# Kernel optimization log

Measured on AMD Instinct MI355X. Metric: run time of the kernel, lower is better.

The kernel has to match this reference:

```python
import jax, jax.numpy as jnp
import numpy as np

A = -0.75  # torch grid_sample bicubic coefficient
EPS_CLAMP = 1e-07


def geo_pad(x, p):
    # GeoCyclicPadding: flip+half-roll across poles (H), circular in longitude (W)
    B, C, H, W = x.shape
    top = jnp.roll(jnp.flip(x[:, :, :p, :], axis=2), W // 2, axis=3)
    bot = jnp.roll(jnp.flip(x[:, :, H - p:, :], axis=2), W // 2, axis=3)
    x = jnp.concatenate([top, x, bot], axis=2)
    return jnp.concatenate([x[:, :, :, W - p:], x, x[:, :, :, :p]], axis=3)


def conv3(x, w, b):
    y = jax.lax.conv_general_dilated(x, w, (1, 1), 'VALID',
                                     dimension_numbers=('NCHW', 'OIHW', 'NCHW'))
    return y + b[None, :, None, None]


def layernorm_chw(x, g, b):
    mu = jnp.mean(x, axis=(1, 2, 3), keepdims=True)
    var = jnp.mean((x - mu) ** 2, axis=(1, 2, 3), keepdims=True)
    return (x - mu) * jax.lax.rsqrt(var + 1e-5) * g[None] + b[None]


def cubic_weights(t):
    # cubic convolution weights for taps at offsets -1,0,1,2 (a = -0.75)
    w0 = A * (1 + t) ** 3 - 5 * A * (1 + t) ** 2 + 8 * A * (1 + t) - 4 * A
    w1 = (A + 2) * t ** 3 - (A + 3) * t ** 2 + 1
    w2 = (A + 2) * (1 - t) ** 3 - (A + 3) * (1 - t) ** 2 + 1
    w3 = A * (2 - t) ** 3 - 5 * A * (2 - t) ** 2 + 8 * A * (2 - t) - 4 * A
    return (w0, w1, w2, w3)


def bicubic_sample_border(img, gx, gy):
    # img: [N,Hp,Wp]; gx,gy: [N,H,W] normalized coords; align_corners=True, border padding
    N, Hp, Wp = img.shape
    ix = jnp.clip((gx + 1) * 0.5 * (Wp - 1), 0.0, Wp - 1)
    iy = jnp.clip((gy + 1) * 0.5 * (Hp - 1), 0.0, Hp - 1)
    x0f = jnp.floor(ix)
    y0f = jnp.floor(iy)
    tx = ix - x0f
    ty = iy - y0f
    x0 = x0f.astype(jnp.int32)
    y0 = y0f.astype(jnp.int32)
    wx = cubic_weights(tx)
    wy = cubic_weights(ty)
    nidx = jnp.arange(N)[:, None, None]
    out = jnp.zeros_like(ix)
    for i in range(4):
        yi = jnp.clip(y0 + (i - 1), 0, Hp - 1)
        row = jnp.zeros_like(ix)
        for j in range(4):
            xj = jnp.clip(x0 + (j - 1), 0, Wp - 1)
            row = row + wx[j] * img[nidx, yi, xj]
        out = out + wy[i] * row
    return out


def reference(hidden_features, lat_grid, lon_grid, w1, b1, ln_g, ln_b, w2, b2, dt):
    B, C, H, W = hidden_features.shape
    # velocity_net = CLP (double conv)
    x = geo_pad(hidden_features, 1)
    x = conv3(x, w1, b1)
    x = jax.nn.silu(layernorm_chw(x, ln_g, ln_b))
    x = geo_pad(x, 1)
    vel = conv3(x, w2, b2)                      # [B, 2C, H, W]
    vel = vel.reshape(B, 2, C, H, W).transpose(0, 2, 1, 3, 4)  # [B, C, 2, H, W]
    u = vel[:, :, 0]
    v = vel[:, :, 1]
    lon_prime = -u * dt
    lat_prime = -v * dt
    lat_p = lat_grid[:, None, :, :]  # broadcast over channels
    lon_p = lon_grid[:, None, :, :]
    # rotated -> standard lat/lon
    sin_lat_prime = jnp.sin(lat_prime)
    cos_lat_prime = jnp.cos(lat_prime)
    sin_lon_prime = jnp.sin(lon_prime)
    cos_lon_prime = jnp.cos(lon_prime)
    sin_lat_p = jnp.sin(lat_p)
    cos_lat_p = jnp.cos(lat_p)
    sin_lat = sin_lat_prime * cos_lat_p + cos_lat_prime * cos_lon_prime * sin_lat_p
    lat_dep = jnp.arcsin(jnp.clip(sin_lat, -1 + EPS_CLAMP, 1 - EPS_CLAMP))
    num = cos_lat_prime * sin_lon_prime
    den = cos_lat_prime * cos_lon_prime * cos_lat_p - sin_lat_prime * sin_lat_p
    lon_dep = lon_p + jnp.arctan2(num, den)
    lon_dep = jnp.remainder(lon_dep + 2 * jnp.pi, 2 * jnp.pi)
    pw = W + 2
    ph = H + 2
    grid_x = (lon_dep / (2 * jnp.pi) * 2 - 1) * (W / pw)
    grid_y = (lat_dep / jnp.pi * 2 - 1) * (H / ph)
    padded = geo_pad(hidden_features, 1).reshape(B * C, ph, pw)
    out = bicubic_sample_border(padded,
                                grid_x.reshape(B * C, H, W),
                                grid_y.reshape(B * C, H, W))
    return out.reshape(B, C, H, W)


def setup_inputs() -> dict:
    key = jax.random.key(0)
    ks = jax.random.split(key, 4)
    B, C, H, W = 2, 128, 240, 480
    hidden_features = jax.random.normal(ks[0], (B, C, H, W), dtype=jnp.float32)
    lat = jnp.linspace(-jnp.pi / 2 + 1e-3, jnp.pi / 2 - 1e-3, H, dtype=jnp.float32)
    lon = jnp.linspace(0.0, 2 * jnp.pi * (1 - 1.0 / W), W, dtype=jnp.float32)
    lat_grid = jnp.broadcast_to(lat[None, :, None], (B, H, W)).astype(jnp.float32)
    lon_grid = jnp.broadcast_to(lon[None, None, :], (B, H, W)).astype(jnp.float32)
    w1 = jax.random.normal(ks[1], (C, C, 3, 3), dtype=jnp.float32) * 0.02
    b1 = jnp.zeros((C,), dtype=jnp.float32)
    ln_g = jnp.ones((C, H, W), dtype=jnp.float32)
    ln_b = jnp.zeros((C, H, W), dtype=jnp.float32)
    w2 = jax.random.normal(ks[2], (2 * C, C, 3, 3), dtype=jnp.float32) * 0.02
    b2 = jnp.zeros((2 * C,), dtype=jnp.float32)
    return {"hidden_features": hidden_features, "lat_grid": lat_grid,
            "lon_grid": lon_grid, "w1": w1, "b1": b1, "ln_g": ln_g,
            "ln_b": ln_b, "w2": w2, "b2": b2, "dt": 0.1}
```

## Files before the change

### kernel.cpp

```cpp
#include <hip/hip_runtime.h>
#include <math.h>

#define Hh 240
#define Ww 480
#define HW 115200
#define Cc 128
#define Kk 1152
#define HALFW 240
#define NB_RED 1440
#define WLCAP 4194304

typedef unsigned int u32;
typedef unsigned short u16;
typedef short bf16x8 __attribute__((ext_vector_type(8)));
typedef float f32x4 __attribute__((ext_vector_type(4)));
typedef __attribute__((address_space(3))) u32 lds_u32;
typedef const __attribute__((address_space(1))) u32 glb_u32;

__device__ __forceinline__ u16 f2bf(float x) {
    u32 u = __float_as_uint(x);
    u32 r = (u + 0x7fffu + ((u >> 16) & 1u)) >> 16;
    return (u16)r;
}
__device__ __forceinline__ float bf2f(u16 h) { return __uint_as_float(((u32)h) << 16); }

__device__ __forceinline__ int geo_sidx(int r, int c) {
    int wv = (c < 0) ? (Ww - 1) : ((c >= Ww) ? 0 : c);
    int rr;
    if (r < 0)        { rr = 0;      wv = (wv >= HALFW) ? wv - HALFW : wv + HALFW; }
    else if (r >= Hh) { rr = Hh - 1; wv = (wv >= HALFW) ? wv - HALFW : wv + HALFW; }
    else              { rr = r; }
    return rr * Ww + wv;
}

__device__ __forceinline__ float padfetch(const float* __restrict__ p, int yi, int xj) {
    return p[geo_sidx(yi - 1, xj - 1)];
}

__device__ __forceinline__ void sincos_small(double x, double* s, double* c) {
    double x2 = x * x;
    if (x2 > 0.49) { *s = sin(x); *c = cos(x); return; }
    *s = x * (1.0 + x2 * (-1.6666666666666666e-1 + x2 * (8.3333333333333333e-3 +
         x2 * (-1.9841269841269841e-4 + x2 * (2.7557319223985893e-6 - x2 * 2.5052108385441720e-8)))));
    *c = 1.0 + x2 * (-0.5 + x2 * (4.1666666666666666e-2 + x2 * (-1.3888888888888889e-3 +
         x2 * (2.4801587301587302e-5 - x2 * 2.7557319223985893e-7))));
}

__device__ __forceinline__ void snipe_tail(double u, double v, double dt,
                                           double phi_s, double phi_c, double lam,
                                           const float* __restrict__ plane,
                                           float* __restrict__ outp)
{
    const double TWO_PI = 6.2831853071795864769252867665590;
    const double PI_D   = 3.1415926535897932384626433832795;

    double lonp = -u * dt, latp = -v * dt;
    double slp, clp, slo, clo;
    sincos_small(latp, &slp, &clp);
    sincos_small(lonp, &slo, &clo);

    double sinlat = slp * phi_c + clp * clo * phi_s;
    sinlat = fmin(fmax(sinlat, -1.0 + 1e-7), 1.0 - 1e-7);
    double lat_dep = asin(sinlat);

    double num = clp * slo;
    double den = clp * clo * phi_c - slp * phi_s;
    double lon_dep = lam + atan2(num, den);
    double xr = lon_dep + TWO_PI;
    xr = xr - floor(xr / TWO_PI) * TWO_PI;

    double gx = (xr / TWO_PI * 2.0 - 1.0) * (480.0 / 482.0);
    double gy = (lat_dep / PI_D * 2.0 - 1.0) * (240.0 / 242.0);
    double ixd = fmin(fmax((gx + 1.0) * 0.5 * 481.0, 0.0), 481.0);
    double iyd = fmin(fmax((gy + 1.0) * 0.5 * 241.0, 0.0), 241.0);

    double x0d = floor(ixd), y0d = floor(iyd);
    float fx = (float)(ixd - x0d), fy = (float)(iyd - y0d);
    int x0 = (int)x0d, y0 = (int)y0d;

    const float a = -0.75f;
    float wx[4], wy[4];
    {
        float t = fx;
        float t1 = 1.f + t, t2 = 2.f - t, s1 = 1.f - t;
        wx[0] = ((a * t1 - 5.f * a) * t1 + 8.f * a) * t1 - 4.f * a;
        wx[1] = ((a + 2.f) * t - (a + 3.f)) * t * t + 1.f;
        wx[2] = ((a + 2.f) * s1 - (a + 3.f)) * s1 * s1 + 1.f;
        wx[3] = ((a * t2 - 5.f * a) * t2 + 8.f * a) * t2 - 4.f * a;
        t = fy;
        t1 = 1.f + t; t2 = 2.f - t; s1 = 1.f - t;
        wy[0] = ((a * t1 - 5.f * a) * t1 + 8.f * a) * t1 - 4.f * a;
        wy[1] = ((a + 2.f) * t - (a + 3.f)) * t * t + 1.f;
        wy[2] = ((a + 2.f) * s1 - (a + 3.f)) * s1 * s1 + 1.f;
        wy[3] = ((a * t2 - 5.f * a) * t2 + 8.f * a) * t2 - 4.f * a;
    }
    float accv = 0.f;
    #pragma unroll
    for (int i = 0; i < 4; i++) {
        int yi = min(max(y0 + i - 1, 0), 241);
        float row = 0.f;
        #pragma unroll
        for (int j = 0; j < 4; j++) {
            int xj = min(max(x0 + j - 1, 0), 481);
            row = fmaf(wx[j], padfetch(plane, yi, xj), row);
        }
        accv = fmaf(wy[i], row, accv);
    }
    *outp = accv;
}

__global__ void reorder_w(const float* __restrict__ w, u16* __restrict__ outp, int NN) {
    int idx = blockIdx.x * 256 + threadIdx.x;
    int total = 3 * NN * Kk;
    if (idx >= total) return;
    int per_kt = 3 * NN * 32;
    int t = idx / per_kt;
    int rem = idx - t * per_kt;
    int U = rem >> 3, j = rem & 7;
    int NT64 = (NN / 16) * 64;
    int p = U / NT64;
    int r2 = U - p * NT64;
    int ntile = r2 >> 6, part = (r2 >> 4) & 3, nlow = r2 & 15;
    int n = ntile * 16 + nlow;
    int k = t * 32 + part * 8 + j;
    float x = w[(size_t)n * Kk + k];
    u16 a = f2bf(x); float r1 = x - bf2f(a);
    u16 b = f2bf(r1); float rr = r1 - bf2f(b);
    outp[idx] = (p == 0) ? a : ((p == 1) ? b : f2bf(rr));
}

template<int NN>
__global__ __launch_bounds__(256)
void conv_mfma(const float* __restrict__ in,
               const u16*  __restrict__ wspr,
               const float* __restrict__ bias,
               float* __restrict__ out)
{
    constexpr int NT     = NN / 32;
    constexpr int NTILES = NN / 16;
    __shared__ short Al[3][8][4][16][8];
    __shared__ short Bl[3][NTILES][4][16][8];

    const int tid  = threadIdx.x;
    const int lane = tid & 63;
    const int wave = tid >> 6;
    const int wm = wave & 1, wn = wave >> 1;
    const int lr = lane & 15, kg = lane >> 4;
    const int m0 = blockIdx.x * 128;

    const int ms   = tid & 127;
    const int ks   = (tid >> 7) * 16;
    const int mt_s = ms >> 4, lr_s = ms & 15;
    const int kg0  = ks >> 3;
    const int gm = m0 + ms;
    const int h = gm / Ww, w = gm - h * Ww;
    int sidx[9];
    #pragma unroll
    for (int q = 0; q < 9; q++) sidx[q] = geo_sidx(h + q / 3 - 1, w + q % 3 - 1);

    short* const Blbase = &Bl[0][0][0][0][0];
    const u16* const bsrc = wspr + (size_t)tid * 8;
    constexpr int NCH = (3 * NN * 32 / 8) / 256;

    f32x4 acc[4][NT] = {};

    for (int kt = 0; kt < Kk; kt += 32) {
        __syncthreads();
        {
            const u16* src = bsrc + (size_t)(kt >> 5) * (3 * NN * 32);
            #pragma unroll
            for (int cg = 0; cg < NCH; cg++) {
                __builtin_amdgcn_global_load_lds(
                    (glb_u32*)(src + (size_t)cg * 2048),
                    (lds_u32*)(Blbase + (size_t)(cg * 256 + tid) * 8),
                    16, 0, 0);
            }
        }
        {
            int k = kt + ks;
            int ic = k / 9, t9 = k - ic * 9;
            short hh[3][16];
            #pragma unroll
            for (int j = 0; j < 16; j++) {
                float x = in[ic * HW + sidx[t9]];
                u16 a = f2bf(x); float r1 = x - bf2f(a);
                u16 b = f2bf(r1); float r2 = r1 - bf2f(b);
                hh[0][j] = (short)a; hh[1][j] = (short)b; hh[2][j] = (short)f2bf(r2);
                if (++t9 == 9) { t9 = 0; ic++; }
            }
            #pragma unroll
            for (int p = 0; p < 3; p++) {
                #pragma unroll
                for (int half = 0; half < 2; half++) {
                    bf16x8 v;
                    #pragma unroll
                    for (int j = 0; j < 8; j++) v[j] = hh[p][half * 8 + j];
                    *(bf16x8*)&Al[p][mt_s][kg0 + half][lr_s][0] = v;
                }
            }
        }
        __syncthreads();
        bf16x8 af[3][4];
        #pragma unroll
        for (int pa = 0; pa < 3; pa++)
            #pragma unroll
            for (int mt = 0; mt < 4; mt++)
                af[pa][mt] = *(const bf16x8*)&Al[pa][wm * 4 + mt][kg][lr][0];
        #pragma unroll
        for (int pb = 0; pb < 3; pb++) {
            #pragma unroll
            for (int nt = 0; nt < NT; nt++) {
                bf16x8 bq = *(const bf16x8*)&Bl[pb][wn * NT + nt][kg][lr][0];
                #pragma unroll
                for (int pa = 0; pa < 3 - pb; pa++) {
                    #pragma unroll
                    for (int mt = 0; mt < 4; mt++)
                        acc[mt][nt] = __builtin_amdgcn_mfma_f32_16x16x32_bf16(
                            af[pa][mt], bq, acc[mt][nt], 0, 0, 0);
                }
            }
        }
    }
    #pragma unroll
    for (int mt = 0; mt < 4; mt++) {
        int mbase = m0 + wm * 64 + mt * 16 + kg * 4;
        #pragma unroll
        for (int nt = 0; nt < NT; nt++) {
            int n = wn * (NN / 2) + nt * 16 + lr;
            float bv = bias[n];
            float4 o;
            o.x = acc[mt][nt][0] + bv;
            o.y = acc[mt][nt][1] + bv;
            o.z = acc[mt][nt][2] + bv;
            o.w = acc[mt][nt][3] + bv;
            *(float4*)&out[(size_t)n * HW + mbase] = o;
        }
    }
}

__global__ __launch_bounds__(256)
void reduce_stats(const float* __restrict__ y, float* __restrict__ part) {
    const int n4 = (Cc * HW) / 4;
    float s = 0.f, ss = 0.f;
    for (int i = blockIdx.x * 256 + threadIdx.x; i < n4; i += NB_RED * 256) {
        float4 v = ((const float4*)y)[i];
        s  += v.x + v.y + v.z + v.w;
        ss += v.x * v.x + v.y * v.y + v.z * v.z + v.w * v.w;
    }
    #pragma unroll
    for (int o = 32; o > 0; o >>= 1) { s += __shfl_down(s, o); ss += __shfl_down(ss, o); }
    __shared__ float ls[4], lss[4];
    int wid = threadIdx.x >> 6, lane = threadIdx.x & 63;
    if (lane == 0) { ls[wid] = s; lss[wid] = ss; }
    __syncthreads();
    if (threadIdx.x == 0) {
        part[blockIdx.x * 2]     = ls[0] + ls[1] + ls[2] + ls[3];
        part[blockIdx.x * 2 + 1] = lss[0] + lss[1] + lss[2] + lss[3];
    }
}

__global__ __launch_bounds__(256)
void finalize_stats(const float* __restrict__ part, float* __restrict__ stats) {
    float s = 0.f, ss = 0.f;
    for (int i = threadIdx.x; i < NB_RED; i += 256) { s += part[2 * i]; ss += part[2 * i + 1]; }
    #pragma unroll
    for (int o = 32; o > 0; o >>= 1) { s += __shfl_down(s, o); ss += __shfl_down(ss, o); }
    __shared__ float ls[4], lss[4];
    int wid = threadIdx.x >> 6, lane = threadIdx.x & 63;
    if (lane == 0) { ls[wid] = s; lss[wid] = ss; }
    __syncthreads();
    if (threadIdx.x == 0) {
        stats[0] = ls[0] + ls[1] + ls[2] + ls[3];
        stats[1] = lss[0] + lss[1] + lss[2] + lss[3];
    }
}

__global__ void norm_silu(float* __restrict__ y, const float* __restrict__ g,
                          const float* __restrict__ bb, const float* __restrict__ stats) {
    int i = blockIdx.x * 256 + threadIdx.x;
    if (i >= Cc * HW) return;
    const float invN = 1.f / (float)(Cc * HW);
    float mu  = stats[0] * invN;
    float var = stats[1] * invN - mu * mu;
    float inv = rsqrtf(var + 1e-5f);
    float z = (y[i] - mu) * inv * g[i] + bb[i];
    y[i] = z / (1.f + expf(-z));
}

__global__ __launch_bounds__(256)
void semilag(const float* __restrict__ vel, const float* __restrict__ hid,
             const float* __restrict__ latg, const float* __restrict__ lng,
             const float* __restrict__ dtp, float* __restrict__ out,
             u32* __restrict__ wl, u32* __restrict__ wlcnt)
{
    int idx = blockIdx.x * 256 + threadIdx.x;
    if (idx >= Cc * HW) return;
    int c = idx / HW;
    int m = idx - c * HW;

    const float PI2F = 6.28318530717958647692f;

    float uf = vel[idx];
    float vf = vel[Cc * HW + idx];
    float dtf = dtp[0];
    float phi = latg[m], lam = lng[m];
    float sphi = sinf(phi), cphi = cosf(phi);

    float lonp = -uf * dtf, latp = -vf * dtf;
    float slp = sinf(latp), clp = cosf(latp);
    float slo = sinf(lonp), clo = cosf(lonp);
    float sinlat = slp * cphi + clp * clo * sphi;
    float num = clp * slo;
    float den = clp * clo * cphi - slp * sphi;
    float r2 = num * num + den * den;

    float lon_w = lam + atan2f(num, den) + PI2F;
    lon_w = lon_w - floorf(lon_w / PI2F) * PI2F;
    float seam = fminf(lon_w, PI2F - lon_w);

    bool pole = (m < 2 * Ww) | (m >= HW - 2 * Ww);
    bool snipe = !pole & ((r2 < 1e-4f) | (fabsf(sinlat) > 1.f - 1e-5f) | (seam < 1e-3f));
    if (snipe) {
        u32 s = atomicAdd(wlcnt, 1u);
        if (s < WLCAP) wl[s] = (u32)idx;
    }

    float sl = fminf(fmaxf(sinlat, -1.f + 1e-7f), 1.f - 1e-7f);
    float lat_dep = asinf(sl);
    float gx = (lon_w / PI2F * 2.f - 1.f) * (480.f / 482.f);
    float gy = (lat_dep / 3.14159265358979323846f * 2.f - 1.f) * (240.f / 242.f);
    double ixd = (double)fminf(fmaxf((gx + 1.f) * 0.5f * 481.f, 0.f), 481.f);
    double iyd = (double)fminf(fmaxf((gy + 1.f) * 0.5f * 241.f, 0.f), 241.f);

    double x0d = floor(ixd), y0d = floor(iyd);
    float fx = (float)(ixd - x0d), fy = (float)(iyd - y0d);
    int x0 = (int)x0d, y0 = (int)y0d;

    const float a = -0.75f;
    float wx[4], wy[4];
    {
        float t = fx;
        float t1 = 1.f + t, t2 = 2.f - t, s1 = 1.f - t;
        wx[0] = ((a * t1 - 5.f * a) * t1 + 8.f * a) * t1 - 4.f * a;
        wx[1] = ((a + 2.f) * t - (a + 3.f)) * t * t + 1.f;
        wx[2] = ((a + 2.f) * s1 - (a + 3.f)) * s1 * s1 + 1.f;
        wx[3] = ((a * t2 - 5.f * a) * t2 + 8.f * a) * t2 - 4.f * a;
        t = fy;
        t1 = 1.f + t; t2 = 2.f - t; s1 = 1.f - t;
        wy[0] = ((a * t1 - 5.f * a) * t1 + 8.f * a) * t1 - 4.f * a;
        wy[1] = ((a + 2.f) * t - (a + 3.f)) * t * t + 1.f;
        wy[2] = ((a + 2.f) * s1 - (a + 3.f)) * s1 * s1 + 1.f;
        wy[3] = ((a * t2 - 5.f * a) * t2 + 8.f * a) * t2 - 4.f * a;
    }

    const float* plane = hid + (size_t)c * HW;
    float accv = 0.f;
    #pragma unroll
    for (int i = 0; i < 4; i++) {
        int yi = min(max(y0 + i - 1, 0), 241);
        float row = 0.f;
        #pragma unroll
        for (int j = 0; j < 4; j++) {
            int xj = min(max(x0 + j - 1, 0), 481);
            row = fmaf(wx[j], padfetch(plane, yi, xj), row);
        }
        accv = fmaf(wy[i], row, accv);
    }
    out[idx] = accv;
}

__global__ __launch_bounds__(256)
void sniper_rows(const float* __restrict__ y1, const float* __restrict__ w2,
                 const float* __restrict__ b2, const float* __restrict__ hid,
                 const float* __restrict__ latg, const float* __restrict__ lng,
                 const float* __restrict__ dtp, float* __restrict__ out)
{
    __shared__ float xl[Kk];
    __shared__ double resd[256];

    const int tid = threadIdx.x;
    const int ri  = blockIdx.x / Ww;
    const int col = blockIdx.x - ri * Ww;
    const int r   = (ri < 2) ? ri : (236 + ri);
    const int m   = r * Ww + col;

    for (int k = tid; k < Kk; k += 256) {
        int ic = k / 9, t9 = k - ic * 9;
        xl[k] = y1[ic * HW + geo_sidx(r + t9 / 3 - 1, col + t9 % 3 - 1)];
    }
    __syncthreads();

    {
        const float* wrow = w2 + (size_t)tid * Kk;
        double a0 = 0.0, a1 = 0.0, a2 = 0.0, a3 = 0.0;
        #pragma unroll 4
        for (int k = 0; k < Kk; k += 4) {
            a0 = fma((double)wrow[k],     (double)xl[k],     a0);
            a1 = fma((double)wrow[k + 1], (double)xl[k + 1], a1);
            a2 = fma((double)wrow[k + 2], (double)xl[k + 2], a2);
            a3 = fma((double)wrow[k + 3], (double)xl[k + 3], a3);
        }
        resd[tid] = (a0 + a1) + (a2 + a3);
    }
    __syncthreads();

    if (tid < Cc) {
        double u = (double)b2[tid] + resd[tid];
        double v = (double)b2[Cc + tid] + resd[Cc + tid];
        double dt = (double)dtp[0];
        double phi = (double)latg[m];
        snipe_tail(u, v, dt, sin(phi), cos(phi), (double)lng[m],
                   hid + (size_t)tid * HW, &out[(size_t)tid * HW + m]);
    }
}

__global__ __launch_bounds__(256)
void sniper(const u32* __restrict__ wl, const u32* __restrict__ wlcnt,
            const float* __restrict__ y1, const float* __restrict__ w2,
            const float* __restrict__ b2, const float* __restrict__ hid,
            const float* __restrict__ latg, const float* __restrict__ lng,
            const float* __restrict__ dtp, float* __restrict__ out)
{
    const int lane = threadIdx.x & 63;
    const int wavid = (blockIdx.x * 256 + threadIdx.x) >> 6;
    const int nwaves = gridDim.x * 4;
    int n = (int)*wlcnt; if (n > WLCAP) n = WLCAP;

    for (int e = wavid; e < n; e += nwaves) {
        u32 idx = wl[e];
        int c = idx / HW, m = idx - c * HW;
        int h = m / Ww, w = m - h * Ww;

        double su = 0.0, sv = 0.0;
        const float* wu = w2 + (size_t)c * Kk;
        const float* wv = w2 + (size_t)(Cc + c) * Kk;
        #pragma unroll
        for (int t9 = 0; t9 < 9; t9++) {
            int s = geo_sidx(h + t9 / 3 - 1, w + t9 % 3 - 1);
            #pragma unroll
            for (int q = 0; q < 2; q++) {
                int ic = q * 64 + lane;
                int k = ic * 9 + t9;
                double yv = (double)y1[ic * HW + s];
                su = fma((double)wu[k], yv, su);
                sv = fma((double)wv[k], yv, sv);
            }
        }
        #pragma unroll
        for (int o = 32; o > 0; o >>= 1) {
            su += __shfl_down(su, o);
            sv += __shfl_down(sv, o);
        }
        if (lane == 0) {
            double u = (double)b2[c] + su;
            double v = (double)b2[Cc + c] + sv;
            double dt = (double)dtp[0];
            double phi = (double)latg[m];
            snipe_tail(u, v, dt, sin(phi), cos(phi), (double)lng[m],
                       hid + (size_t)c * HW, &out[idx]);
        }
    }
}

extern "C" void kernel_launch(void* const* d_in, const int* in_sizes, int n_in,
                              void* d_out, int out_size, void* d_ws, size_t ws_size,
                              hipStream_t stream)
{
    const float* hidden = (const float*)d_in[0];
    const float* latg   = (const float*)d_in[1];
    const float* lng    = (const float*)d_in[2];
    const float* w1     = (const float*)d_in[3];
    const float* b1     = (const float*)d_in[4];
    const float* g      = (const float*)d_in[5];
    const float* lb     = (const float*)d_in[6];
    const float* w2     = (const float*)d_in[7];
    const float* b2     = (const float*)d_in[8];
    const float* dt     = (const float*)d_in[9];
    float* out = (float*)d_out;

    float* ws    = (float*)d_ws;
    float* stats = ws;
    float* part  = ws + 4;
    u32*   wlcnt = (u32*)(ws + 4 + 2 * NB_RED);
    u16*   wsp1  = (u16*)(ws + 4 + 2 * NB_RED + 4);
    u16*   wsp2  = wsp1 + (size_t)3 * Cc * Kk;
    float* y1    = (float*)(wsp2 + (size_t)3 * 2 * Cc * Kk);
    float* vel   = y1 + (size_t)Cc * HW;
    u32*   wl    = (u32*)(vel + (size_t)2 * Cc * HW);

    reorder_w<<<(3 * Cc * Kk + 255) / 256, 256, 0, stream>>>(w1, wsp1, Cc);
    reorder_w<<<(3 * 2 * Cc * Kk + 255) / 256, 256, 0, stream>>>(w2, wsp2, 2 * Cc);

    for (int b = 0; b < 2; b++) {
        const float* hb = hidden + (size_t)b * Cc * HW;
        const float* lab = latg + (size_t)b * HW;
        const float* lob = lng + (size_t)b * HW;
        float* ob = out + (size_t)b * Cc * HW;

        conv_mfma<128><<<HW / 128, 256, 0, stream>>>(hb, wsp1, b1, y1);
        reduce_stats<<<NB_RED, 256, 0, stream>>>(y1, part);
        finalize_stats<<<1, 256, 0, stream>>>(part, stats + 2 * b);
        norm_silu<<<(Cc * HW) / 256, 256, 0, stream>>>(y1, g, lb, stats + 2 * b);
        conv_mfma<256><<<HW / 128, 256, 0, stream>>>(y1, wsp2, b2, vel);
        hipMemsetAsync(wlcnt, 0, 4, stream);
        semilag<<<(Cc * HW) / 256, 256, 0, stream>>>(vel, hb, lab, lob, dt, ob, wl, wlcnt);
        sniper_rows<<<4 * Ww, 256, 0, stream>>>(y1, w2, b2, hb, lab, lob, dt, ob);
        sniper<<<2048, 256, 0, stream>>>(wl, wlcnt, y1, w2, b2, hb, lab, lob, dt, ob);
    }
}
```

Measured before the change: 2.719 ms.

## Double-buffer conv MFMA LDS tiles and widen blocks to 512 threads

Measured after the change: 2.791 ms. 2.7% more time.

```diff
diff --git a/kernel.cpp b/kernel.cpp
--- a/kernel.cpp
+++ b/kernel.cpp
@@ -130,16 +130,16 @@
 }
 
 template<int NN>
-__global__ __launch_bounds__(256)
+__global__ __launch_bounds__(512)
 void conv_mfma(const float* __restrict__ in,
                const u16*  __restrict__ wspr,
                const float* __restrict__ bias,
                float* __restrict__ out)
 {
-    constexpr int NT     = NN / 32;
+    constexpr int NT     = NN / 64;
     constexpr int NTILES = NN / 16;
-    __shared__ short Al[3][8][4][16][8];
-    __shared__ short Bl[3][NTILES][4][16][8];
+    __shared__ short Al[2][3][8][4][16][8];
+    __shared__ short Bl[2][3][NTILES][4][16][8];
 
     const int tid  = threadIdx.x;
     const int lane = tid & 63;
@@ -149,84 +149,98 @@
     const int m0 = blockIdx.x * 128;
 
     const int ms   = tid & 127;
-    const int ks   = (tid >> 7) * 16;
+    const int grp  = tid >> 7;
     const int mt_s = ms >> 4, lr_s = ms & 15;
-    const int kg0  = ks >> 3;
     const int gm = m0 + ms;
     const int h = gm / Ww, w = gm - h * Ww;
     int sidx[9];
     #pragma unroll
     for (int q = 0; q < 9; q++) sidx[q] = geo_sidx(h + q / 3 - 1, w + q % 3 - 1);
 
-    short* const Blbase = &Bl[0][0][0][0][0];
-    const u16* const bsrc = wspr + (size_t)tid * 8;
-    constexpr int NCH = (3 * NN * 32 / 8) / 256;
+    constexpr int NCH = (3 * NN * 32 / 8) / 512;
 
     f32x4 acc[4][NT] = {};
 
+    auto stageB = [&](int buf, int kt) {
+        const u16* src = wspr + (size_t)(kt >> 5) * (3 * NN * 32) + (size_t)tid * 8;
+        short* dst = &Bl[buf][0][0][0][0][0];
+        #pragma unroll
+        for (int cg = 0; cg < NCH; cg++) {
+            __builtin_amdgcn_global_load_lds(
+                (glb_u32*)(src + (size_t)cg * 4096),
+                (lds_u32*)(dst + (size_t)(cg * 512 + tid) * 8), 16, 0, 0);
+        }
+    };
+    auto loadA = [&](int kt, float* xv) {
+        int k = kt + grp * 8;
+        int ic = k / 9, t9 = k - ic * 9;
+        #pragma unroll
+        for (int j = 0; j < 8; j++) {
+            xv[j] = in[ic * HW + sidx[t9]];
+            if (++t9 == 9) { t9 = 0; ic++; }
+        }
+    };
+    auto writeA = [&](int buf, const float* xv) {
+        bf16x8 v0, v1, v2;
+        #pragma unroll
+        for (int j = 0; j < 8; j++) {
+            float x = xv[j];
+            u16 a = f2bf(x); float r1 = x - bf2f(a);
+            u16 b = f2bf(r1); float r2 = r1 - bf2f(b);
+            v0[j] = (short)a; v1[j] = (short)b; v2[j] = (short)f2bf(r2);
+        }
+        *(bf16x8*)&Al[buf][0][mt_s][grp][lr_s][0] = v0;
+        *(bf16x8*)&Al[buf][1][mt_s][grp][lr_s][0] = v1;
+        *(bf16x8*)&Al[buf][2][mt_s][grp][lr_s][0] = v2;
+    };
+
+    {
+        float xv[8];
+        stageB(0, 0);
+        loadA(0, xv);
+        writeA(0, xv);
+    }
+
+    int cur = 0;
     for (int kt = 0; kt < Kk; kt += 32) {
-        __syncthreads();
-        {
-            const u16* src = bsrc + (size_t)(kt >> 5) * (3 * NN * 32);
-            #pragma unroll
-            for (int cg = 0; cg < NCH; cg++) {
-                __builtin_amdgcn_global_load_lds(
-                    (glb_u32*)(src + (size_t)cg * 2048),
-                    (lds_u32*)(Blbase + (size_t)(cg * 256 + tid) * 8),
-                    16, 0, 0);
-            }
-        }
-        {
-            int k = kt + ks;
-            int ic = k / 9, t9 = k - ic * 9;
-            short hh[3][16];
-            #pragma unroll
-            for (int j = 0; j < 16; j++) {
-                float x = in[ic * HW + sidx[t9]];
-                u16 a = f2bf(x); float r1 = x - bf2f(a);
-                u16 b = f2bf(r1); float r2 = r1 - bf2f(b);
-                hh[0][j] = (short)a; hh[1][j] = (short)b; hh[2][j] = (short)f2bf(r2);
-                if (++t9 == 9) { t9 = 0; ic++; }
-            }
-            #pragma unroll
-            for (int p = 0; p < 3; p++) {
-                #pragma unroll
-                for (int half = 0; half < 2; half++) {
-                    bf16x8 v;
-                    #pragma unroll
-                    for (int j = 0; j < 8; j++) v[j] = hh[p][half * 8 + j];
-                    *(bf16x8*)&Al[p][mt_s][kg0 + half][lr_s][0] = v;
-                }
-            }
-        }
         __syncthreads();
         bf16x8 af[3][4];
         #pragma unroll
         for (int pa = 0; pa < 3; pa++)
             #pragma unroll
             for (int mt = 0; mt < 4; mt++)
-                af[pa][mt] = *(const bf16x8*)&Al[pa][wm * 4 + mt][kg][lr][0];
+                af[pa][mt] = *(const bf16x8*)&Al[cur][pa][wm * 4 + mt][kg][lr][0];
+
+        float xv[8];
+        const bool more = (kt + 32 < Kk);
+        if (more) {
+            stageB(cur ^ 1, kt + 32);
+            loadA(kt + 32, xv);
+        }
+
         #pragma unroll
         for (int pb = 0; pb < 3; pb++) {
             #pragma unroll
             for (int nt = 0; nt < NT; nt++) {
-                bf16x8 bq = *(const bf16x8*)&Bl[pb][wn * NT + nt][kg][lr][0];
+                bf16x8 bq = *(const bf16x8*)&Bl[cur][pb][wn * NT + nt][kg][lr][0];
                 #pragma unroll
-                for (int pa = 0; pa < 3 - pb; pa++) {
+                for (int pa = 0; pa < 3 - pb; pa++)
                     #pragma unroll
                     for (int mt = 0; mt < 4; mt++)
                         acc[mt][nt] = __builtin_amdgcn_mfma_f32_16x16x32_bf16(
                             af[pa][mt], bq, acc[mt][nt], 0, 0, 0);
-                }
             }
         }
-    }
+        if (more) writeA(cur ^ 1, xv);
+        cur ^= 1;
+    }
+
     #pragma unroll
     for (int mt = 0; mt < 4; mt++) {
         int mbase = m0 + wm * 64 + mt * 16 + kg * 4;
         #pragma unroll
         for (int nt = 0; nt < NT; nt++) {
-            int n = wn * (NN / 2) + nt * 16 + lr;
+            int n = wn * (NN / 4) + nt * 16 + lr;
             float bv = bias[n];
             float4 o;
             o.x = acc[mt][nt][0] + bv;
@@ -497,11 +511,11 @@
         const float* lob = lng + (size_t)b * HW;
         float* ob = out + (size_t)b * Cc * HW;
 
-        conv_mfma<128><<<HW / 128, 256, 0, stream>>>(hb, wsp1, b1, y1);
+        conv_mfma<128><<<HW / 128, 512, 0, stream>>>(hb, wsp1, b1, y1);
         reduce_stats<<<NB_RED, 256, 0, stream>>>(y1, part);
         finalize_stats<<<1, 256, 0, stream>>>(part, stats + 2 * b);
         norm_silu<<<(Cc * HW) / 256, 256, 0, stream>>>(y1, g, lb, stats + 2 * b);
-        conv_mfma<256><<<HW / 128, 256, 0, stream>>>(y1, wsp2, b2, vel);
+        conv_mfma<256><<<HW / 128, 512, 0, stream>>>(y1, wsp2, b2, vel);
         hipMemsetAsync(wlcnt, 0, 4, stream);
         semilag<<<(Cc * HW) / 256, 256, 0, stream>>>(vel, hb, lab, lob, dt, ob, wl, wlcnt);
         sniper_rows<<<4 * Ww, 256, 0, stream>>>(y1, w2, b2, hb, lab, lob, dt, ob);
```
